# Performance work log

Measured on AMD Instinct MI355X. Metric: run time of the kernel, lower is better.

Reference implementation:

```python
import jax, jax.numpy as jnp
import numpy as np

B, S, H, OUT = 512, 128, 512, 1
IN = 1
P = 0.1  # drop_rate


def setup_inputs() -> dict:
    key = jax.random.key(0)
    ks = jax.random.split(key, 14)
    x = jax.random.normal(ks[0], (B, S), dtype=jnp.float32)
    # Bayesian LSTM variational params (blitz-style: W = mu + log1p(exp(rho)) * eps)
    W_ih_mu = jax.random.normal(ks[1], (IN, 4 * H), dtype=jnp.float32) * 0.1
    W_ih_rho = jnp.full((IN, 4 * H), -5.0, dtype=jnp.float32)
    eps_ih = jax.random.normal(ks[2], (IN, 4 * H), dtype=jnp.float32)
    W_hh_mu = jax.random.normal(ks[3], (H, 4 * H), dtype=jnp.float32) * 0.1
    W_hh_rho = jnp.full((H, 4 * H), -5.0, dtype=jnp.float32)
    eps_hh = jax.random.normal(ks[4], (H, 4 * H), dtype=jnp.float32)
    b_mu = jax.random.normal(ks[5], (4 * H,), dtype=jnp.float32) * 0.1
    b_rho = jnp.full((4 * H,), -5.0, dtype=jnp.float32)
    eps_b = jax.random.normal(ks[6], (4 * H,), dtype=jnp.float32)
    # linear head
    W_lin = jax.random.normal(ks[7], (H, OUT), dtype=jnp.float32) * 0.05
    b_lin = jnp.zeros((OUT,), dtype=jnp.float32)
    # dropout masks (training=True always); pre-scaled inverted dropout
    keep = 1.0 - P
    mask_in = jax.random.bernoulli(ks[8], keep, (B, S, 1)).astype(jnp.float32) / keep
    # second dropout is applied to hidden_seq then sliced at t=-1, so only the
    # last-step mask matters
    mask_out = jax.random.bernoulli(ks[9], keep, (B, H)).astype(jnp.float32) / keep
    return {
        "x": x,
        "W_ih_mu": W_ih_mu, "W_ih_rho": W_ih_rho, "eps_ih": eps_ih,
        "W_hh_mu": W_hh_mu, "W_hh_rho": W_hh_rho, "eps_hh": eps_hh,
        "b_mu": b_mu, "b_rho": b_rho, "eps_b": eps_b,
        "W_lin": W_lin, "b_lin": b_lin,
        "mask_in": mask_in, "mask_out": mask_out,
    }


def reference(x, W_ih_mu, W_ih_rho, eps_ih, W_hh_mu, W_hh_rho, eps_hh,
              b_mu, b_rho, eps_b, W_lin, b_lin, mask_in, mask_out):
    # reparameterized weight samples
    W_ih = W_ih_mu + jnp.log1p(jnp.exp(W_ih_rho)) * eps_ih   # (IN, 4H)
    W_hh = W_hh_mu + jnp.log1p(jnp.exp(W_hh_rho)) * eps_hh   # (H, 4H)
    b = b_mu + jnp.log1p(jnp.exp(b_rho)) * eps_b             # (4H,)

    # reshape (B,S) -> (B,S,1) + input dropout
    xr = x[:, :, None] * mask_in                              # (B,S,1)
    # input projection for all timesteps at once
    x_proj = jnp.einsum('bsi,ih->bsh', xr, W_ih) + b          # (B,S,4H)
    xs = jnp.swapaxes(x_proj, 0, 1)                           # (S,B,4H)

    h0 = jnp.zeros((B, H), dtype=x.dtype)
    c0 = jnp.zeros((B, H), dtype=x.dtype)

    def step(carry, gx):
        h, c = carry
        gates = gx + h @ W_hh                                 # (B,4H)
        i_g, f_g, g_g, o_g = jnp.split(gates, 4, axis=-1)
        i_t = jax.nn.sigmoid(i_g)
        f_t = jax.nn.sigmoid(f_g)
        g_t = jnp.tanh(g_g)
        o_t = jax.nn.sigmoid(o_g)
        c_new = f_t * c + i_t * g_t
        h_new = o_t * jnp.tanh(c_new)
        return (h_new, c_new), h_new

    (h_last, _), _ = jax.lax.scan(step, (h0, c0), xs)
    # output dropout (only last step matters after slicing), then linear head
    out = (h_last * mask_out) @ W_lin + b_lin                 # (B,OUT)
    return out
```

## Files before the change

### kernel.cpp

```cpp
#include <hip/hip_runtime.h>
#include <hip/hip_bf16.h>


typedef __attribute__((ext_vector_type(8))) _Float16 half8;
typedef __attribute__((ext_vector_type(4))) float f32x4;
typedef unsigned long long u64;
typedef unsigned int u32;

#define HID   512
#define BATCH 512
#define SEQ   128

__device__ __forceinline__ float bf2f(__hip_bfloat16 v) { return __bfloat162float(v); }
__device__ __forceinline__ float softplus_f(float x) { return log1pf(__expf(x)); }
__device__ __forceinline__ float sigm(float x) { return 1.f / (1.f + __expf(-x)); }
__device__ __forceinline__ float tanh_fast(float x) {
  x = fminf(fmaxf(x, -15.f), 15.f);
  float e = __expf(2.f * x);
  return (e - 1.f) / (e + 1.f);
}
__device__ __forceinline__ float ldin(const void* p, size_t i, int md) {
  return md ? ((const float*)p)[i] : bf2f(((const __hip_bfloat16*)p)[i]);
}
__device__ __forceinline__ int probe_md(const void* b_rho) {
  return (((const u32*)b_rho)[0] == 0xC0A00000u) ? 1 : 0;
}
__device__ __forceinline__ unsigned short f16bits(_Float16 h) {
  union { _Float16 f; unsigned short u; } c; c.f = h; return c.u;
}
__device__ __forceinline__ u64 ald64(const u64* p) {
  return __hip_atomic_load((u64*)p, __ATOMIC_RELAXED, __HIP_MEMORY_SCOPE_AGENT);
}
__device__ __forceinline__ u32 ald32(const u32* p) {
  return __hip_atomic_load((u32*)p, __ATOMIC_RELAXED, __HIP_MEMORY_SCOPE_AGENT);
}
__device__ __forceinline__ void ast32(u32* p, u32 v) {
  (void)__hip_atomic_exchange(p, v, __ATOMIC_RELAXED, __HIP_MEMORY_SCOPE_AGENT);
}
__device__ __forceinline__ void ast64(u64* p, u64 v) {
  (void)__hip_atomic_exchange(p, v, __ATOMIC_RELAXED, __HIP_MEMORY_SCOPE_AGENT);
}

__device__ __forceinline__ void pollR13(const u32* p, u32 tgt) {
  long gd = 0;
  for (;;) {
    const u32 v = ald32(p);
    if (__ballot(v >= tgt) == ~0ULL) break;
    if (++gd > 1000000L) break;
  }
}

__global__ __launch_bounds__(256) void setup_all(
    const void* __restrict__ x,
    const void* __restrict__ Wih_mu, const void* __restrict__ Wih_rho,
    const void* __restrict__ eps_ih,
    const void* __restrict__ Whh_mu, const void* __restrict__ Whh_rho,
    const void* __restrict__ eps_hh,
    const void* __restrict__ b_mu, const void* __restrict__ b_rho,
    const void* __restrict__ eps_b,
    const void* __restrict__ mask_in,
    unsigned short* __restrict__ Wtf,
    float* __restrict__ Wih4, float* __restrict__ bias4, float* __restrict__ xm,
    u32* __restrict__ hA32, u32* __restrict__ flags) {
  const int md = probe_md(b_rho);
  const int bid = blockIdx.x;
  if (bid < 512) {
    const int idx = bid * 256 + threadIdx.x;
    const int ncol = idx & 2047;
    const int kq = idx >> 11;
    const int kk = kq >> 2, q = kq & 3;
    const int g = ncol >> 9, j = ncol & 511;
    const int js = j >> 4, rr = j & 15;
    const int lane = rr + 16 * q;
    union { half8 h; unsigned short s[8]; } out;
#pragma unroll
    for (int s = 0; s < 8; ++s) {
      const size_t src = (size_t)(kk * 32 + q * 8 + s) * 2048 + ncol;
      const float w = ldin(Whh_mu, src, md) +
                      softplus_f(ldin(Whh_rho, src, md)) * ldin(eps_hh, src, md);
      out.s[s] = f16bits((_Float16)w);
    }
    *(half8*)(Wtf + (((size_t)((g * 32 + js) * 16 + kk) * 64 + lane) * 8)) = out.h;
  } else {
    const int idx = (bid - 512) * 256 + threadIdx.x;
    if (idx < 2048) {
      Wih4[idx] = ldin(Wih_mu, idx, md) +
                  softplus_f(ldin(Wih_rho, idx, md)) * ldin(eps_ih, idx, md);
    } else if (idx < 4096) {
      const int n = idx - 2048;
      bias4[n] = ldin(b_mu, n, md) + softplus_f(ldin(b_rho, n, md)) * ldin(eps_b, n, md);
    } else if (idx < 69632) {
      const int i = idx - 4096;
      const int s = i >> 9, b = i & 511;
      const size_t src = (size_t)b * SEQ + s;
      xm[(size_t)s * BATCH + b] = ldin(x, src, md) * ldin(mask_in, src, md);
    } else if (idx < 200704) {
      hA32[idx - 69632] = 0u;
    } else if (idx < 204800) {
      flags[idx - 200704] = 0u;
    }
  }
}

__global__ __launch_bounds__(512, 2) void lstm_persist(
    u64* __restrict__ hA, u64* __restrict__ hB,
    float* __restrict__ hf, const unsigned short* __restrict__ Wtf,
    const float* __restrict__ Wih4, const float* __restrict__ bias4,
    const float* __restrict__ xm, u32* __restrict__ flags,
    const void* __restrict__ mask_out, const void* __restrict__ W_lin,
    const void* __restrict__ b_lin, const void* __restrict__ b_rho,
    void* __restrict__ out) {
  __shared__ half8 WS[2048];
  __shared__ f32x4 exch[8][4][64];
  __shared__ u32 T[4][16][17];
  const int tid  = threadIdx.x;
  const int lane = tid & 63;
  const int wv   = tid >> 6;
  const int w    = wv & 3;
  const int hv   = wv >> 2;
  const int r = lane & 15, q = lane >> 4;
  const int bid = blockIdx.x;
  const int mg = bid >> 5, js = bid & 31;
  const int j0 = js * 16, m0 = mg * 64 + w * 16, mt = mg * 4 + w;
  const int md = probe_md(b_rho);

  for (int fi = tid; fi < 2048; fi += 512) {
    const int wsg = fi >> 10;
    const int kk = (fi >> 6) & 15;
    const int ln = fi & 63;
    WS[fi] = *(const half8*)(
        Wtf + (((size_t)(((wsg + 2) * 32 + js) * 16 + kk) * 64 + ln) * 8));
  }
  half8 breg[2][8];
#pragma unroll
  for (int g = 0; g < 2; ++g)
#pragma unroll
    for (int kkl = 0; kkl < 8; ++kkl)
      breg[g][kkl] = *(const half8*)(
          Wtf + (((size_t)((g * 32 + js) * 16 + hv * 8 + kkl) * 64 + lane) * 8));
  __syncthreads();

  const int jj = j0 + r;
  const float wih_i = Wih4[jj],             bi  = bias4[jj];
  const float wih_f = Wih4[HID + jj],       bfv = bias4[HID + jj];
  const float wih_g = Wih4[2 * HID + jj],   bg  = bias4[2 * HID + jj];
  const float wih_o = Wih4[3 * HID + jj],   bo  = bias4[3 * HID + jj];

  float cc0 = 0.f, cc1 = 0.f;
  u32* myflag = flags + (size_t)(mg * 32 + js) * 16;
  u32* pollp  = flags + (size_t)(mg * 32 + (lane & 31)) * 16;

  const int mtc = wv >> 1, half = wv & 1;
  const int sl = lane & 31;
  const int sri = sl & 15;
  const int sc0 = ((sl >> 4) << 3) + half * 4;
  const size_t oidx = (size_t)((mg * 4 + mtc) * 16 + (js >> 1)) * 128 +
                      (size_t)half * 64 + (size_t)(js & 1) * 32 + sl;

  for (int t = 0; t < SEQ; ++t) {
    const u64* ih = (t & 1) ? hB : hA;
    u64*       oh = (t & 1) ? hA : hB;

    const size_t rb = (size_t)(mt * 16 + hv * 8) * 128 + lane;
    u64 uh[16];
#pragma unroll
    for (int kkl = 0; kkl < 8; ++kkl) {
      uh[kkl * 2]     = ald64(ih + rb + (size_t)kkl * 128);
      uh[kkl * 2 + 1] = ald64(ih + rb + (size_t)kkl * 128 + 64);
    }

    const float xb0 = xm[t * BATCH + m0 + q * 4 + hv * 2 + 0];
    const float xb1 = xm[t * BATCH + m0 + q * 4 + hv * 2 + 1];

    f32x4 a0 = {0.f, 0.f, 0.f, 0.f};
    f32x4 a1 = a0, a2 = a0, a3 = a0;
#pragma unroll
    for (int kkl = 0; kkl < 8; ++kkl) {
      const int kk = hv * 8 + kkl;
      const half8 b2 = WS[(0 * 16 + kk) * 64 + lane];
      const half8 b3 = WS[(1 * 16 + kk) * 64 + lane];
      union { half8 h; u64 d[2]; } ah;
      ah.d[0] = uh[kkl * 2]; ah.d[1] = uh[kkl * 2 + 1];
      a0 = __builtin_amdgcn_mfma_f32_16x16x32_f16(ah.h, breg[0][kkl], a0, 0, 0, 0);
      a1 = __builtin_amdgcn_mfma_f32_16x16x32_f16(ah.h, breg[1][kkl], a1, 0, 0, 0);
      a2 = __builtin_amdgcn_mfma_f32_16x16x32_f16(ah.h, b2, a2, 0, 0, 0);
      a3 = __builtin_amdgcn_mfma_f32_16x16x32_f16(ah.h, b3, a3, 0, 0, 0);
    }

    exch[wv][0][lane] = a0; exch[wv][1][lane] = a1;
    exch[wv][2][lane] = a2; exch[wv][3][lane] = a3;
    __syncthreads();
    const int pw = wv ^ 4;
    a0 += exch[pw][0][lane]; a1 += exch[pw][1][lane];
    a2 += exch[pw][2][lane]; a3 += exch[pw][3][lane];

#pragma unroll
    for (int i2 = 0; i2 < 2; ++i2) {
      const int i = hv * 2 + i2;
      const int m = m0 + q * 4 + i;
      const float xb = i2 ? xb1 : xb0;
      const float pi = a0[i] + xb * wih_i + bi;
      const float pf = a1[i] + xb * wih_f + bfv;
      const float pg = a2[i] + xb * wih_g + bg;
      const float po = a3[i] + xb * wih_o + bo;
      const float cprev = i2 ? cc1 : cc0;
      const float cn = sigm(pf) * cprev + sigm(pi) * tanh_fast(pg);
      const float hn = sigm(po) * tanh_fast(cn);
      if (i2) cc1 = cn; else cc0 = cn;
      T[w][q * 4 + i][r] = (u32)f16bits((_Float16)hn);
      if (t == SEQ - 1)
        ast32((u32*)(hf + (size_t)m * HID + jj), __float_as_uint(hn));
    }
    __syncthreads();

    if (lane < 32) {
      const u32 x0 = T[mtc][sri][sc0];
      const u32 x1 = T[mtc][sri][sc0 + 1];
      const u32 x2 = T[mtc][sri][sc0 + 2];
      const u32 x3 = T[mtc][sri][sc0 + 3];
      const u64 hv64 = (u64)((x0 & 0xffffu) | (x1 << 16)) |
                       ((u64)((x2 & 0xffffu) | (x3 << 16)) << 32);
      ast64(oh + oidx, hv64);
    }

    if (t < SEQ - 1) {
      __syncthreads();
      if (tid == 0) ast32(myflag, (u32)(t + 1));
      if (wv == 0) pollR13(pollp, (u32)(t + 1));
      __syncthreads();
    }
  }

  __syncthreads();
  if (tid == 0) ast32(myflag, (u32)SEQ);
  if (wv == 0) pollR13(pollp, (u32)SEQ);
  __syncthreads();

  const int rA = mg * 64 + js * 2;
  const size_t iA = (size_t)rA * HID + tid;
  const size_t iB = iA + HID;
  const float hAv = __uint_as_float(ald32((const u32*)hf + iA));
  const float hBv = __uint_as_float(ald32((const u32*)hf + iB));
  float sA = hAv * ldin(mask_out, iA, md) * ldin(W_lin, tid, md);
  float sB = hBv * ldin(mask_out, iB, md) * ldin(W_lin, tid, md);
#pragma unroll
  for (int off = 32; off; off >>= 1) {
    sA += __shfl_down(sA, off, 64);
    sB += __shfl_down(sB, off, 64);
  }
  float* red = (float*)&T[0][0][0];
  if (lane == 0) { red[wv] = sA; red[8 + wv] = sB; }
  __syncthreads();
  if (tid == 0) {
    const float tA = ((red[0] + red[1]) + (red[2] + red[3])) +
                     ((red[4] + red[5]) + (red[6] + red[7]));
    const float tB = ((red[8] + red[9]) + (red[10] + red[11])) +
                     ((red[12] + red[13]) + (red[14] + red[15]));
    const float bl = ldin(b_lin, 0, md);
    if (md) {
      ((float*)out)[rA]     = tA + bl;
      ((float*)out)[rA + 1] = tB + bl;
    } else {
      ((__hip_bfloat16*)out)[rA]     = __float2bfloat16(tA + bl);
      ((__hip_bfloat16*)out)[rA + 1] = __float2bfloat16(tB + bl);
    }
  }
}

extern "C" void kernel_launch(void* const* d_in, const int* in_sizes, int n_in,
                              void* d_out, int out_size, void* d_ws, size_t ws_size,
                              hipStream_t stream) {
  const void* x        = d_in[0];
  const void* Wih_mu   = d_in[1];
  const void* Wih_rho  = d_in[2];
  const void* eps_ih   = d_in[3];
  const void* Whh_mu   = d_in[4];
  const void* Whh_rho  = d_in[5];
  const void* eps_hh   = d_in[6];
  const void* b_mu     = d_in[7];
  const void* b_rho    = d_in[8];
  const void* eps_b    = d_in[9];
  const void* W_lin    = d_in[10];
  const void* b_lin    = d_in[11];
  const void* mask_in  = d_in[12];
  const void* mask_out = d_in[13];

  char* ws = (char*)d_ws;
  unsigned short* Wtf = (unsigned short*)(ws);
  float* Wih4  = (float*)(ws + 2097152);
  float* bias4 = (float*)(ws + 2105344);
  float* xm    = (float*)(ws + 2113536);
  u64*   hA    = (u64*)(ws + 2375680);
  u64*   hB    = (u64*)(ws + 2899968);
  float* hf    = (float*)(ws + 3424256);
  u32*   flags = (u32*)(ws + 4472832);

  setup_all<<<1312, 256, 0, stream>>>(x, Wih_mu, Wih_rho, eps_ih,
                                      Whh_mu, Whh_rho, eps_hh,
                                      b_mu, b_rho, eps_b, mask_in,
                                      Wtf, Wih4, bias4, xm, (u32*)hA, flags);

  void* outp = d_out;
  void* kargs[] = {&hA, &hB, &hf, &Wtf, &Wih4, &bias4, &xm, &flags,
                   (void*)&mask_out, (void*)&W_lin, (void*)&b_lin,
                   (void*)&b_rho, &outp};
  hipLaunchCooperativeKernel(reinterpret_cast<void*>(&lstm_persist),
                             dim3(256), dim3(512), kargs, 0, stream);
}
```

Before: 603.6 us.

## Fuse weight reparameterization and input masking into persistent LSTM kernel

Removes the separate setup kernel. Each persistent block now computes its own slice of the sampled recurrent weights, input weights and bias directly from mu/rho/eps, and stages the masked input for its batch rows in shared memory. The h buffer and flags are zeroed with memsets instead. This saves a kernel launch and the workspace round trip, and turns per-step global xm loads into LDS reads. In exchange each block does strided, uncoalesced global reads of the raw weights and redundant softplus work in its prologue, and adds about 33KB of LDS, which may pressure occupancy at 2 blocks per CU.

```diff
diff --git a/kernel.cpp b/kernel.cpp
--- a/kernel.cpp
+++ b/kernel.cpp
@@ -50,69 +50,27 @@
   }
 }
 
-__global__ __launch_bounds__(256) void setup_all(
-    const void* __restrict__ x,
+__device__ __forceinline__ float reparam(const void* mu, const void* rho,
+                                         const void* eps, size_t i, int md) {
+  return ldin(mu, i, md) + softplus_f(ldin(rho, i, md)) * ldin(eps, i, md);
+}
+
+__global__ __launch_bounds__(512, 2) void lstm_persist(
+    u64* __restrict__ hA, u64* __restrict__ hB,
+    float* __restrict__ hf, u32* __restrict__ flags,
+    const void* __restrict__ x, const void* __restrict__ mask_in,
     const void* __restrict__ Wih_mu, const void* __restrict__ Wih_rho,
     const void* __restrict__ eps_ih,
     const void* __restrict__ Whh_mu, const void* __restrict__ Whh_rho,
     const void* __restrict__ eps_hh,
     const void* __restrict__ b_mu, const void* __restrict__ b_rho,
     const void* __restrict__ eps_b,
-    const void* __restrict__ mask_in,
-    unsigned short* __restrict__ Wtf,
-    float* __restrict__ Wih4, float* __restrict__ bias4, float* __restrict__ xm,
-    u32* __restrict__ hA32, u32* __restrict__ flags) {
-  const int md = probe_md(b_rho);
-  const int bid = blockIdx.x;
-  if (bid < 512) {
-    const int idx = bid * 256 + threadIdx.x;
-    const int ncol = idx & 2047;
-    const int kq = idx >> 11;
-    const int kk = kq >> 2, q = kq & 3;
-    const int g = ncol >> 9, j = ncol & 511;
-    const int js = j >> 4, rr = j & 15;
-    const int lane = rr + 16 * q;
-    union { half8 h; unsigned short s[8]; } out;
-#pragma unroll
-    for (int s = 0; s < 8; ++s) {
-      const size_t src = (size_t)(kk * 32 + q * 8 + s) * 2048 + ncol;
-      const float w = ldin(Whh_mu, src, md) +
-                      softplus_f(ldin(Whh_rho, src, md)) * ldin(eps_hh, src, md);
-      out.s[s] = f16bits((_Float16)w);
-    }
-    *(half8*)(Wtf + (((size_t)((g * 32 + js) * 16 + kk) * 64 + lane) * 8)) = out.h;
-  } else {
-    const int idx = (bid - 512) * 256 + threadIdx.x;
-    if (idx < 2048) {
-      Wih4[idx] = ldin(Wih_mu, idx, md) +
-                  softplus_f(ldin(Wih_rho, idx, md)) * ldin(eps_ih, idx, md);
-    } else if (idx < 4096) {
-      const int n = idx - 2048;
-      bias4[n] = ldin(b_mu, n, md) + softplus_f(ldin(b_rho, n, md)) * ldin(eps_b, n, md);
-    } else if (idx < 69632) {
-      const int i = idx - 4096;
-      const int s = i >> 9, b = i & 511;
-      const size_t src = (size_t)b * SEQ + s;
-      xm[(size_t)s * BATCH + b] = ldin(x, src, md) * ldin(mask_in, src, md);
-    } else if (idx < 200704) {
-      hA32[idx - 69632] = 0u;
-    } else if (idx < 204800) {
-      flags[idx - 200704] = 0u;
-    }
-  }
-}
-
-__global__ __launch_bounds__(512, 2) void lstm_persist(
-    u64* __restrict__ hA, u64* __restrict__ hB,
-    float* __restrict__ hf, const unsigned short* __restrict__ Wtf,
-    const float* __restrict__ Wih4, const float* __restrict__ bias4,
-    const float* __restrict__ xm, u32* __restrict__ flags,
     const void* __restrict__ mask_out, const void* __restrict__ W_lin,
-    const void* __restrict__ b_lin, const void* __restrict__ b_rho,
-    void* __restrict__ out) {
+    const void* __restrict__ b_lin, void* __restrict__ out) {
   __shared__ half8 WS[2048];
   __shared__ f32x4 exch[8][4][64];
   __shared__ u32 T[4][16][17];
+  __shared__ float xmL[64][129];
   const int tid  = threadIdx.x;
   const int lane = tid & 63;
   const int wv   = tid >> 6;
@@ -124,27 +82,50 @@
   const int j0 = js * 16, m0 = mg * 64 + w * 16, mt = mg * 4 + w;
   const int md = probe_md(b_rho);
 
+  for (int i = tid; i < 8192; i += 512) {
+    const int bl = i >> 7, s = i & 127;
+    const size_t src = (size_t)(mg * 64 + bl) * SEQ + s;
+    xmL[bl][s] = ldin(x, src, md) * ldin(mask_in, src, md);
+  }
   for (int fi = tid; fi < 2048; fi += 512) {
     const int wsg = fi >> 10;
     const int kk = (fi >> 6) & 15;
     const int ln = fi & 63;
-    WS[fi] = *(const half8*)(
-        Wtf + (((size_t)(((wsg + 2) * 32 + js) * 16 + kk) * 64 + ln) * 8));
+    const int rr2 = ln & 15, q2 = ln >> 4;
+    const int ncol = (wsg + 2) * 512 + js * 16 + rr2;
+    union { half8 h; unsigned short sb[8]; } o;
+#pragma unroll
+    for (int s = 0; s < 8; ++s) {
+      const size_t src = (size_t)(kk * 32 + q2 * 8 + s) * 2048 + ncol;
+      o.sb[s] = f16bits((_Float16)reparam(Whh_mu, Whh_rho, eps_hh, src, md));
+    }
+    WS[fi] = o.h;
   }
   half8 breg[2][8];
 #pragma unroll
   for (int g = 0; g < 2; ++g)
 #pragma unroll
-    for (int kkl = 0; kkl < 8; ++kkl)
-      breg[g][kkl] = *(const half8*)(
-          Wtf + (((size_t)((g * 32 + js) * 16 + hv * 8 + kkl) * 64 + lane) * 8));
-  __syncthreads();
-
+    for (int kkl = 0; kkl < 8; ++kkl) {
+      const int kk = hv * 8 + kkl;
+      const int ncol = g * 512 + js * 16 + r;
+      union { half8 h; unsigned short sb[8]; } o;
+#pragma unroll
+      for (int s = 0; s < 8; ++s) {
+        const size_t src = (size_t)(kk * 32 + q * 8 + s) * 2048 + ncol;
+        o.sb[s] = f16bits((_Float16)reparam(Whh_mu, Whh_rho, eps_hh, src, md));
+      }
+      breg[g][kkl] = o.h;
+    }
   const int jj = j0 + r;
-  const float wih_i = Wih4[jj],             bi  = bias4[jj];
-  const float wih_f = Wih4[HID + jj],       bfv = bias4[HID + jj];
-  const float wih_g = Wih4[2 * HID + jj],   bg  = bias4[2 * HID + jj];
-  const float wih_o = Wih4[3 * HID + jj],   bo  = bias4[3 * HID + jj];
+  const float wih_i = reparam(Wih_mu, Wih_rho, eps_ih, jj, md);
+  const float wih_f = reparam(Wih_mu, Wih_rho, eps_ih, 512 + jj, md);
+  const float wih_g = reparam(Wih_mu, Wih_rho, eps_ih, 1024 + jj, md);
+  const float wih_o = reparam(Wih_mu, Wih_rho, eps_ih, 1536 + jj, md);
+  const float bi  = reparam(b_mu, b_rho, eps_b, jj, md);
+  const float bfv = reparam(b_mu, b_rho, eps_b, 512 + jj, md);
+  const float bg  = reparam(b_mu, b_rho, eps_b, 1024 + jj, md);
+  const float bo  = reparam(b_mu, b_rho, eps_b, 1536 + jj, md);
+  __syncthreads();
 
   float cc0 = 0.f, cc1 = 0.f;
   u32* myflag = flags + (size_t)(mg * 32 + js) * 16;
@@ -157,6 +138,8 @@
   const size_t oidx = (size_t)((mg * 4 + mtc) * 16 + (js >> 1)) * 128 +
                       (size_t)half * 64 + (size_t)(js & 1) * 32 + sl;
 
+  const int bl0 = w * 16 + q * 4 + hv * 2;
+
   for (int t = 0; t < SEQ; ++t) {
     const u64* ih = (t & 1) ? hB : hA;
     u64*       oh = (t & 1) ? hA : hB;
@@ -169,8 +152,8 @@
       uh[kkl * 2 + 1] = ald64(ih + rb + (size_t)kkl * 128 + 64);
     }
 
-    const float xb0 = xm[t * BATCH + m0 + q * 4 + hv * 2 + 0];
-    const float xb1 = xm[t * BATCH + m0 + q * 4 + hv * 2 + 1];
+    const float xb0 = xmL[bl0][t];
+    const float xb1 = xmL[bl0 + 1][t];
 
     f32x4 a0 = {0.f, 0.f, 0.f, 0.f};
     f32x4 a1 = a0, a2 = a0, a3 = a0;
@@ -286,24 +269,21 @@
   const void* mask_out = d_in[13];
 
   char* ws = (char*)d_ws;
-  unsigned short* Wtf = (unsigned short*)(ws);
-  float* Wih4  = (float*)(ws + 2097152);
-  float* bias4 = (float*)(ws + 2105344);
-  float* xm    = (float*)(ws + 2113536);
-  u64*   hA    = (u64*)(ws + 2375680);
-  u64*   hB    = (u64*)(ws + 2899968);
-  float* hf    = (float*)(ws + 3424256);
-  u32*   flags = (u32*)(ws + 4472832);
-
-  setup_all<<<1312, 256, 0, stream>>>(x, Wih_mu, Wih_rho, eps_ih,
-                                      Whh_mu, Whh_rho, eps_hh,
-                                      b_mu, b_rho, eps_b, mask_in,
-                                      Wtf, Wih4, bias4, xm, (u32*)hA, flags);
+  u64*   hA    = (u64*)(ws);
+  u64*   hB    = (u64*)(ws + 524288);
+  float* hf    = (float*)(ws + 1048576);
+  u32*   flags = (u32*)(ws + 2097152);
+
+  hipMemsetAsync(hA, 0, 524288, stream);
+  hipMemsetAsync(flags, 0, 16384, stream);
 
   void* outp = d_out;
-  void* kargs[] = {&hA, &hB, &hf, &Wtf, &Wih4, &bias4, &xm, &flags,
-                   (void*)&mask_out, (void*)&W_lin, (void*)&b_lin,
-                   (void*)&b_rho, &outp};
+  void* kargs[] = {&hA, &hB, &hf, &flags,
+                   (void*)&x, (void*)&mask_in,
+                   (void*)&Wih_mu, (void*)&Wih_rho, (void*)&eps_ih,
+                   (void*)&Whh_mu, (void*)&Whh_rho, (void*)&eps_hh,
+                   (void*)&b_mu, (void*)&b_rho, (void*)&eps_b,
+                   (void*)&mask_out, (void*)&W_lin, (void*)&b_lin, &outp};
   hipLaunchCooperativeKernel(reinterpret_cast<void*>(&lstm_persist),
                              dim3(256), dim3(512), kargs, 0, stream);
 }
```

After: 1.163 ms. 1.93x slower.
